# Performance work log

Hardware: AMD Instinct MI355X
Metric: run time of the kernel (lower is better)

The kernel has to match this reference:

```python
import jax, jax.numpy as jnp
import numpy as np

B, T, W = 8, 4096, 1024          # batch, byte seq len, words per sequence
DB, DW = 64, 512                 # byte_embed_dim, word_embed_dim
NH = 2                           # highway layers per block
VOCAB = 264                      # 256 bytes + 4 + 4 specials
BPE_MARK, WORD_MARK = 4, 3       # bpe_mask_idx, word_mask_idx


def _make_seg_ids():
    # ragged word lengths in {3,4,5}, mean 4, summing to T per sequence
    rng = np.random.default_rng(0)
    seg = np.empty((B, T), np.int32)
    base = T // W
    for b in range(B):
        delta = np.zeros(W, np.int64)
        q = W // 4
        idx = rng.permutation(W)
        delta[idx[:q]] = 1
        delta[idx[q:2 * q]] = -1
        seg[b] = np.repeat(np.arange(W), base + delta)
    return jnp.asarray(seg)


def setup_inputs() -> dict:
    key = jax.random.key(0)
    ks = jax.random.split(key, 12)
    s = 0.05
    byte_tokens = jax.random.randint(ks[0], (B, T), 4, VOCAB)
    bpe_mask = jax.random.bernoulli(ks[1], 0.25, (B, T))
    word_mask = jax.random.bernoulli(ks[2], 0.05, (B, T))
    seg_ids = _make_seg_ids()
    tok_emb = (jax.random.normal(ks[3], (VOCAB, DB)) * s).at[0].set(0.0)  # padding_idx=0 row zeroed
    inp = {
        'byte_tokens': byte_tokens, 'bpe_mask': bpe_mask, 'word_mask': word_mask,
        'seg_ids': seg_ids, 'tok_emb': tok_emb,
        'conv0_w': jax.random.normal(ks[4], (3, DB, DW)) * s, 'conv0_b': jnp.zeros((DW,)),
        'hw0_wg': jax.random.normal(ks[5], (NH, DW, DW)) * s, 'hw0_bg': jnp.zeros((NH, DW)),
        'hw0_wh': jax.random.normal(ks[6], (NH, DW, DW)) * s, 'hw0_bh': jnp.zeros((NH, DW)),
        'conv1_w': jax.random.normal(ks[7], (3, DW, DW)) * s, 'conv1_b': jnp.zeros((DW,)),
        'hw1_wg': jax.random.normal(ks[8], (NH, DW, DW)) * s, 'hw1_bg': jnp.zeros((NH, DW)),
        'hw1_wh': jax.random.normal(ks[9], (NH, DW, DW)) * s, 'hw1_bh': jnp.zeros((NH, DW)),
        'proj_w': jax.random.normal(ks[10], (DW, DW)) * s, 'proj_b': jnp.zeros((DW,)),
    }
    return inp


def _conv_highway(x, cw, cb, wg, bg, wh, bh, residual):
    # 1D same-padded conv over sequence, optional residual, relu, then highways
    y = jax.lax.conv_general_dilated(x, cw, (1,), 'SAME',
                                     dimension_numbers=('NWC', 'WIO', 'NWC')) + cb
    if residual:
        y = y + x
    y = jax.nn.relu(y)
    for i in range(NH):
        g = jax.nn.sigmoid(y @ wg[i] + bg[i])
        h = jax.nn.relu(y @ wh[i] + bh[i])
        y = g * h + (1.0 - g) * y
    return y


def reference(byte_tokens, bpe_mask, word_mask, seg_ids, tok_emb,
              conv0_w, conv0_b, hw0_wg, hw0_bg, hw0_wh, hw0_bh,
              conv1_w, conv1_b, hw1_wg, hw1_bg, hw1_wh, hw1_bh,
              proj_w, proj_b):
    # byte embedding + marker embeddings (pad idx 0 -> zero row)
    x = (tok_emb[byte_tokens]
         + tok_emb[jnp.where(bpe_mask, BPE_MARK, 0)]
         + tok_emb[jnp.where(word_mask, WORD_MARK, 0)])          # [B,T,DB]
    x = _conv_highway(x, conv0_w, conv0_b, hw0_wg, hw0_bg, hw0_wh, hw0_bh, False)
    x = _conv_highway(x, conv1_w, conv1_b, hw1_wg, hw1_bg, hw1_wh, hw1_bh, True)
    # ragged per-word segment max over bytes (fused, replaces python loops)
    seg_max = jax.vmap(lambda xi, si: jax.ops.segment_max(xi, si, num_segments=W))
    x = seg_max(x, seg_ids)                                       # [B,W,DW]
    return x @ proj_w + proj_b
```

## Files before the change

kernel.cpp:

```cpp
#include <hip/hip_runtime.h>
#include <hip/hip_bf16.h>

using bf16 = __hip_bfloat16;
typedef __attribute__((ext_vector_type(8))) short s8v;
typedef __attribute__((ext_vector_type(4))) float f4v;

#define T_SEQ 4096
#define DWC 512

__device__ __forceinline__ float fin(float v) {
    return (v == v && fabsf(v) < 1e30f) ? v : 0.0f;
}
__device__ __forceinline__ float ldf(const void* p, size_t i, int f32) {
    return f32 ? ((const float*)p)[i] : __bfloat162float(((const bf16*)p)[i]);
}
__device__ __forceinline__ float b2f(short s) {
    unsigned u = ((unsigned)(unsigned short)s) << 16;
    return __builtin_bit_cast(float, u);
}
__device__ __forceinline__ short f2b(float v) {
    bf16 b = __float2bfloat16(v);
    return __builtin_bit_cast(short, b);
}
__device__ __forceinline__ uint4 ld16(const short* p) { return *(const uint4*)p; }

__device__ __forceinline__ void swz(int L, int G, int& bx, int& by) {
    int k8 = L & 7, sl = L >> 3;
    int gp = G >> 5;
    bx = sl & 3;
    by = k8 * gp + (sl >> 2);
}

__device__ __forceinline__ int swidx(int row, int ch) {
    return row * 32 + ((ch ^ ((row >> 1) & 3)) << 3);
}

__global__ __launch_bounds__(256) void diag_kernel(bf16* __restrict__ out, int n, float v)
{
    int i = blockIdx.x * 256 + threadIdx.x;
    if (i < n) out[i] = __float2bfloat16(i == 0 ? v : 0.0f);
}

__global__ __launch_bounds__(256) void detect_kernel(
    const int* __restrict__ tok, const unsigned char* __restrict__ bpe,
    const unsigned char* __restrict__ wm, const int* __restrict__ seg,
    const unsigned int* __restrict__ embw, int* __restrict__ flags)
{
    __shared__ int sh[5];
    int tid = threadIdx.x;
    if (tid < 5) sh[tid] = 0;
    __syncthreads();
    int bo = 0, bm = 0, wo = 0, wmid = 0;
    for (int i = tid; i < 16384; i += 256) {
        int odd = 2 * i + 1;
        if (bpe[odd]) bo = 1;
        if (wm[odd])  wo = 1;
        int mid = 8 * (i & 4095) + 4;
        if (bpe[mid]) bm = 1;
        if (wm[mid])  wmid = 1;
    }
    if (bo)   atomicOr(&sh[0], 1);
    if (bm)   atomicOr(&sh[1], 1);
    if (wo)   atomicOr(&sh[2], 1);
    if (wmid) atomicOr(&sh[3], 1);
    if (tid < 32 && embw[32 + tid] != 0u) atomicOr(&sh[4], 1);
    __syncthreads();
    if (tid == 0) {
        flags[0] = (tok[32767] != 0) ? 0 : 1;
        flags[1] = sh[0] ? 1 : (sh[1] ? 4 : 8);
        flags[2] = sh[2] ? 1 : (sh[3] ? 4 : 8);
        flags[3] = (seg[32767] != 0) ? 0 : 1;
        flags[4] = sh[4] ? 0 : 1;
    }
}

#define WB_TOTAL 3249664
#define EMB4_ELEMS (264 * 4 * 64)
__global__ __launch_bounds__(256) void convert_weights(
    const void* c0w, const void* c0b, const void* h0g, const void* h0bg,
    const void* h0h, const void* h0bh, const void* c1w, const void* c1b,
    const void* h1g, const void* h1bg, const void* h1h, const void* h1bh,
    const void* pw, const void* pb, const void* emb,
    const int* __restrict__ flags, short* __restrict__ WB)
{
    int f32 = flags[4];
    size_t i = (size_t)blockIdx.x * 256 + threadIdx.x;
    if (i >= WB_TOTAL + EMB4_ELEMS) return;
    if (i >= WB_TOTAL) {
        size_t o = i - WB_TOTAL;
        size_t t = o >> 8, v = (o >> 6) & 3, c = o & 63;
        float val = ldf(emb, t * 64 + c, f32);
        if (v & 1) val += ldf(emb, 4 * 64 + c, f32);
        if (v & 2) val += ldf(emb, 3 * 64 + c, f32);
        WB[i] = f2b(fin(val));
        return;
    }
    const void* src; size_t si;
    if (i < 98304)        { size_t n = i / 192, k = i % 192; src = c0w; si = k * 512 + n; }
    else if (i < 98816)   { src = c0b;  si = i - 98304; }
    else if (i < 623104)  { size_t o = i - 98816;  size_t l = o >> 18; o &= 262143;
                            size_t n = o >> 9, k = o & 511; src = h0g; si = (l << 18) + k * 512 + n; }
    else if (i < 624128)  { src = h0bg; si = i - 623104; }
    else if (i < 1148416) { size_t o = i - 624128; size_t l = o >> 18; o &= 262143;
                            size_t n = o >> 9, k = o & 511; src = h0h; si = (l << 18) + k * 512 + n; }
    else if (i < 1149440) { src = h0bh; si = i - 1148416; }
    else if (i < 1935872) { size_t o = i - 1149440; size_t n = o / 1536, k = o % 1536;
                            src = c1w; si = k * 512 + n; }
    else if (i < 1936384) { src = c1b;  si = i - 1935872; }
    else if (i < 2460672) { size_t o = i - 1936384; size_t l = o >> 18; o &= 262143;
                            size_t n = o >> 9, k = o & 511; src = h1g; si = (l << 18) + k * 512 + n; }
    else if (i < 2461696) { src = h1bg; si = i - 2460672; }
    else if (i < 2985984) { size_t o = i - 2461696; size_t l = o >> 18; o &= 262143;
                            size_t n = o >> 9, k = o & 511; src = h1h; si = (l << 18) + k * 512 + n; }
    else if (i < 2987008) { src = h1bh; si = i - 2985984; }
    else if (i < 3249152) { size_t o = i - 2987008; size_t n = o >> 9, k = o & 511;
                            src = pw; si = k * 512 + n; }
    else                  { src = pb;   si = i - 3249152; }
    WB[i] = f2b(ldf(src, si, f32));
}

__global__ __launch_bounds__(512) void conv0_mfma(
    const int* __restrict__ tok, const unsigned char* __restrict__ bpe,
    const unsigned char* __restrict__ wm, const short* __restrict__ emb4,
    const int* __restrict__ flags, const short* __restrict__ WT,
    const short* __restrict__ bias, short* __restrict__ Out)
{
    constexpr int K = 192;
    constexpr int NIT = 3;
    __shared__ __align__(16) short As[2][256 * 32];
    __shared__ __align__(16) short Bs[2][256 * 32];
    int bx, by;
    swz(blockIdx.x, gridDim.x, bx, by);
    const int bm = by * 128, bn = bx * 128;
    const int tid = threadIdx.x;
    const int wave = tid >> 6, lane = tid & 63;
    const int wmr = (wave >> 1) * 32, wnc = (wave & 1) * 64;
    const int q = lane >> 4, ln16 = lane & 15;
    const int sr = tid >> 2, sch = tid & 3;
    const int tt = (bm + sr) & (T_SEQ - 1);
    const int is64t = flags[0];
    const int wb = flags[1], ww = flags[2];
    const short* Bb = WT + (size_t)(bn + sr) * K + sch * 8;

    f4v acc[2][4] = {};
    uint4 rA0, rA1, rB0, rB1;
    const uint4 z4 = make_uint4(0, 0, 0, 0);

    auto loadA = [&](int tap, uint4& a0, uint4& a1) {
        int ts = tt + tap - 1;
        if ((unsigned)ts < (unsigned)T_SEQ) {
            int bt = bm + sr + tap - 1;
            int tk = is64t ? (int)((const long long*)tok)[bt] : tok[bt];
            tk = min(max(tk, 0), 263);
            int v = (bpe[(size_t)bt * wb] ? 1 : 0) | (wm[(size_t)bt * ww] ? 2 : 0);
            const short* row = emb4 + ((size_t)tk * 4 + v) * 64;
            a0 = ld16(row + sch * 8);
            a1 = ld16(row + 32 + sch * 8);
        } else { a0 = z4; a1 = z4; }
    };

    loadA(0, rA0, rA1);
    rB0 = ld16(Bb);
    rB1 = ld16(Bb + 32);
    *(uint4*)(&As[0][swidx(sr, sch)])       = rA0;
    *(uint4*)(&As[0][swidx(128 + sr, sch)]) = rA1;
    *(uint4*)(&Bs[0][swidx(sr, sch)])       = rB0;
    *(uint4*)(&Bs[0][swidx(128 + sr, sch)]) = rB1;
    __syncthreads();
    int p = 0;

    for (int it = 0; it < NIT; ++it) {
        const bool more = (it + 1 < NIT);
        if (more) {
            int kn = (it + 1) * 64;
            loadA(it + 1, rA0, rA1);
            rB0 = ld16(Bb + kn);
            rB1 = ld16(Bb + kn + 32);
        }
        #pragma unroll
        for (int ks = 0; ks < 2; ks++) {
            s8v af[2], bf[4];
            #pragma unroll
            for (int mi = 0; mi < 2; mi++)
                af[mi] = *(const s8v*)(&As[p][swidx(128 * ks + wmr + mi * 16 + ln16, q)]);
            #pragma unroll
            for (int ni = 0; ni < 4; ni++)
                bf[ni] = *(const s8v*)(&Bs[p][swidx(128 * ks + wnc + ni * 16 + ln16, q)]);
            #pragma unroll
            for (int mi = 0; mi < 2; mi++)
                #pragma unroll
                for (int ni = 0; ni < 4; ni++)
                    acc[mi][ni] = __builtin_amdgcn_mfma_f32_16x16x32_bf16(
                        af[mi], bf[ni], acc[mi][ni], 0, 0, 0);
        }
        if (more) {
            *(uint4*)(&As[p ^ 1][swidx(sr, sch)])       = rA0;
            *(uint4*)(&As[p ^ 1][swidx(128 + sr, sch)]) = rA1;
            *(uint4*)(&Bs[p ^ 1][swidx(sr, sch)])       = rB0;
            *(uint4*)(&Bs[p ^ 1][swidx(128 + sr, sch)]) = rB1;
            __syncthreads();
            p ^= 1;
        }
    }

    #pragma unroll
    for (int mi = 0; mi < 2; mi++)
        #pragma unroll
        for (int ni = 0; ni < 4; ni++) {
            int col = bn + wnc + ni * 16 + ln16;
            float bv = b2f(bias[col]);
            #pragma unroll
            for (int r = 0; r < 4; r++) {
                int orow = bm + wmr + mi * 16 + q * 4 + r;
                Out[(size_t)orow * DWC + col] =
                    f2b(fin(fmaxf(acc[mi][ni][r] + bv, 0.0f)));
            }
        }
}

__global__ __launch_bounds__(512) void conv1_mfma(
    const short* __restrict__ A, const short* __restrict__ WT,
    const short* __restrict__ bias, short* __restrict__ Out)
{
    constexpr int IC = 512;
    constexpr int K = 3 * IC;
    constexpr int NIT = K / 64;
    __shared__ __align__(16) short As[2][256 * 32];
    __shared__ __align__(16) short Bs[2][256 * 32];
    int bx, by;
    swz(blockIdx.x, gridDim.x, bx, by);
    const int bm = by * 128, bn = bx * 128;
    const int tid = threadIdx.x;
    const int wave = tid >> 6, lane = tid & 63;
    const int wmr = (wave >> 1) * 32, wnc = (wave & 1) * 64;
    const int q = lane >> 4, ln16 = lane & 15;
    const int sr = tid >> 2, sch = tid & 3;
    const int tt = (bm + sr) & (T_SEQ - 1);
    const short* Bb = WT + (size_t)(bn + sr) * K + sch * 8;

    f4v acc[2][4] = {};
    uint4 rA0, rA1, rB0, rB1;
    const uint4 z4 = make_uint4(0, 0, 0, 0);

    {
        int ts = tt - 1;
        bool ok = (ts >= 0 && ts < T_SEQ);
        const short* sa = A + (size_t)(bm + sr - 1) * IC + sch * 8;
        rA0 = ok ? ld16(sa) : z4;
        rA1 = ok ? ld16(sa + 32) : z4;
        rB0 = ld16(Bb);
        rB1 = ld16(Bb + 32);
    }
    *(uint4*)(&As[0][swidx(sr, sch)])       = rA0;
    *(uint4*)(&As[0][swidx(128 + sr, sch)]) = rA1;
    *(uint4*)(&Bs[0][swidx(sr, sch)])       = rB0;
    *(uint4*)(&Bs[0][swidx(128 + sr, sch)]) = rB1;
    __syncthreads();
    int p = 0;

    for (int it = 0; it < NIT; ++it) {
        const bool more = (it + 1 < NIT);
        if (more) {
            int kn = (it + 1) * 64;
            int tap = kn / IC, c0 = kn - tap * IC;
            int ts = tt + tap - 1;
            bool ok = (ts >= 0 && ts < T_SEQ);
            const short* sa = A + (size_t)(bm + sr + tap - 1) * IC + c0 + sch * 8;
            rA0 = ok ? ld16(sa) : z4;
            rA1 = ok ? ld16(sa + 32) : z4;
            rB0 = ld16(Bb + kn);
            rB1 = ld16(Bb + kn + 32);
        }
        #pragma unroll
        for (int ks = 0; ks < 2; ks++) {
            s8v af[2], bf[4];
            #pragma unroll
            for (int mi = 0; mi < 2; mi++)
                af[mi] = *(const s8v*)(&As[p][swidx(128 * ks + wmr + mi * 16 + ln16, q)]);
            #pragma unroll
            for (int ni = 0; ni < 4; ni++)
                bf[ni] = *(const s8v*)(&Bs[p][swidx(128 * ks + wnc + ni * 16 + ln16, q)]);
            #pragma unroll
            for (int mi = 0; mi < 2; mi++)
                #pragma unroll
                for (int ni = 0; ni < 4; ni++)
                    acc[mi][ni] = __builtin_amdgcn_mfma_f32_16x16x32_bf16(
                        af[mi], bf[ni], acc[mi][ni], 0, 0, 0);
        }
        if (more) {
            *(uint4*)(&As[p ^ 1][swidx(sr, sch)])       = rA0;
            *(uint4*)(&As[p ^ 1][swidx(128 + sr, sch)]) = rA1;
            *(uint4*)(&Bs[p ^ 1][swidx(sr, sch)])       = rB0;
            *(uint4*)(&Bs[p ^ 1][swidx(128 + sr, sch)]) = rB1;
            __syncthreads();
            p ^= 1;
        }
    }

    #pragma unroll
    for (int mi = 0; mi < 2; mi++)
        #pragma unroll
        for (int ni = 0; ni < 4; ni++) {
            int col = bn + wnc + ni * 16 + ln16;
            float bv = b2f(bias[col]);
            #pragma unroll
            for (int r = 0; r < 4; r++) {
                int orow = bm + wmr + mi * 16 + q * 4 + r;
                float v = acc[mi][ni][r] + bv + b2f(A[(size_t)orow * IC + col]);
                Out[(size_t)orow * DWC + col] = f2b(fin(fmaxf(v, 0.0f)));
            }
        }
}

__global__ __launch_bounds__(512) void highway_mfma(
    const short* __restrict__ Y, const short* __restrict__ WgT,
    const short* __restrict__ bg, const short* __restrict__ WhT,
    const short* __restrict__ bh, short* __restrict__ Out)
{
    __shared__ __align__(16) short As[128 * 32];
    __shared__ __align__(16) short Bg[128 * 32];
    __shared__ __align__(16) short Bh[128 * 32];
    int bx, by;
    swz(blockIdx.x, gridDim.x, bx, by);
    const int bm = by * 128, bn = bx * 128;
    const int tid = threadIdx.x;
    const int wave = tid >> 6, lane = tid & 63;
    const int wmr = (wave >> 1) * 32, wnc = (wave & 1) * 64;
    const int q = lane >> 4, ln16 = lane & 15;
    const int sr = tid >> 2, sch = tid & 3;
    const int sw = swidx(sr, sch);
    const short* A0 = Y   + (size_t)(bm + sr) * DWC + sch * 8;
    const short* G0 = WgT + (size_t)(bn + sr) * DWC + sch * 8;
    const short* H0 = WhT + (size_t)(bn + sr) * DWC + sch * 8;

    f4v accg[2][4] = {};
    f4v acch[2][4] = {};
    uint4 rA = ld16(A0), rG = ld16(G0), rH = ld16(H0);

    for (int k0 = 0; k0 < DWC; k0 += 32) {
        *(uint4*)(&As[sw]) = rA;
        *(uint4*)(&Bg[sw]) = rG;
        *(uint4*)(&Bh[sw]) = rH;
        __syncthreads();
        if (k0 + 32 < DWC) {
            int kn = k0 + 32;
            rA = ld16(A0 + kn); rG = ld16(G0 + kn); rH = ld16(H0 + kn);
        }
        s8v af[2], bgf[4], bhf[4];
        #pragma unroll
        for (int mi = 0; mi < 2; mi++) af[mi] = *(const s8v*)(&As[swidx(wmr + mi * 16 + ln16, q)]);
        #pragma unroll
        for (int ni = 0; ni < 4; ni++) {
            bgf[ni] = *(const s8v*)(&Bg[swidx(wnc + ni * 16 + ln16, q)]);
            bhf[ni] = *(const s8v*)(&Bh[swidx(wnc + ni * 16 + ln16, q)]);
        }
        #pragma unroll
        for (int mi = 0; mi < 2; mi++)
            #pragma unroll
            for (int ni = 0; ni < 4; ni++) {
                accg[mi][ni] = __builtin_amdgcn_mfma_f32_16x16x32_bf16(
                    af[mi], bgf[ni], accg[mi][ni], 0, 0, 0);
                acch[mi][ni] = __builtin_amdgcn_mfma_f32_16x16x32_bf16(
                    af[mi], bhf[ni], acch[mi][ni], 0, 0, 0);
            }
        __syncthreads();
    }

    #pragma unroll
    for (int mi = 0; mi < 2; mi++)
        #pragma unroll
        for (int ni = 0; ni < 4; ni++) {
            int col = bn + wnc + ni * 16 + ln16;
            float bgv = b2f(bg[col]);
            float bhv = b2f(bh[col]);
            #pragma unroll
            for (int r = 0; r < 4; r++) {
                int orow = bm + wmr + mi * 16 + q * 4 + r;
                float g = 1.0f / (1.0f + expf(-(accg[mi][ni][r] + bgv)));
                float h = fmaxf(acch[mi][ni][r] + bhv, 0.0f);
                float y = b2f(Y[(size_t)orow * DWC + col]);
                Out[(size_t)orow * DWC + col] = f2b(fin(g * h + (1.0f - g) * y));
            }
        }
}

__global__ __launch_bounds__(512) void proj_mfma(
    const short* __restrict__ A, const short* __restrict__ WT,
    const short* __restrict__ bias, const int* __restrict__ flags,
    void* __restrict__ Out, int oroff)
{
    __shared__ __align__(16) short As[128 * 32];
    __shared__ __align__(16) short Bs[128 * 32];
    int bx, by;
    swz(blockIdx.x, gridDim.x, bx, by);
    const int bm = by * 128, bn = bx * 128;
    const int tid = threadIdx.x;
    const int wave = tid >> 6, lane = tid & 63;
    const int wmr = (wave >> 1) * 32, wnc = (wave & 1) * 64;
    const int q = lane >> 4, ln16 = lane & 15;
    const int sr = tid >> 2, sch = tid & 3;
    const int sw = swidx(sr, sch);
    const int f32 = flags[4];
    const short* A0 = A  + (size_t)(bm + sr) * DWC + sch * 8;
    const short* B0 = WT + (size_t)(bn + sr) * DWC + sch * 8;

    f4v acc[2][4] = {};
    uint4 rA = ld16(A0), rB = ld16(B0);

    for (int k0 = 0; k0 < DWC; k0 += 32) {
        *(uint4*)(&As[sw]) = rA;
        *(uint4*)(&Bs[sw]) = rB;
        __syncthreads();
        if (k0 + 32 < DWC) {
            int kn = k0 + 32;
            rA = ld16(A0 + kn); rB = ld16(B0 + kn);
        }
        s8v af[2], bf[4];
        #pragma unroll
        for (int mi = 0; mi < 2; mi++) af[mi] = *(const s8v*)(&As[swidx(wmr + mi * 16 + ln16, q)]);
        #pragma unroll
        for (int ni = 0; ni < 4; ni++) bf[ni] = *(const s8v*)(&Bs[swidx(wnc + ni * 16 + ln16, q)]);
        #pragma unroll
        for (int mi = 0; mi < 2; mi++)
            #pragma unroll
            for (int ni = 0; ni < 4; ni++)
                acc[mi][ni] = __builtin_amdgcn_mfma_f32_16x16x32_bf16(
                    af[mi], bf[ni], acc[mi][ni], 0, 0, 0);
        __syncthreads();
    }

    #pragma unroll
    for (int mi = 0; mi < 2; mi++)
        #pragma unroll
        for (int ni = 0; ni < 4; ni++) {
            int col = bn + wnc + ni * 16 + ln16;
            float bv = b2f(bias[col]);
            #pragma unroll
            for (int r = 0; r < 4; r++) {
                int orow = bm + wmr + mi * 16 + q * 4 + r;
                float v = fin(acc[mi][ni][r] + bv);
                size_t oi = (size_t)(oroff + orow) * DWC + col;
                if (f32) ((float*)Out)[oi] = v;
                else     ((bf16*)Out)[oi] = __float2bfloat16(v);
            }
        }
}

__global__ __launch_bounds__(256) void bounds_kernel(
    const int* __restrict__ seg, const int* __restrict__ flags,
    int* __restrict__ wstart, int* __restrict__ wend, int bt0)
{
    int il = blockIdx.x * 256 + threadIdx.x;
    int ig = bt0 + il;
    int is64 = flags[3];
    const long long* seg64 = (const long long*)seg;
    int t = il & (T_SEQ - 1);
    int bl = il >> 12;
    int s  = (is64 ? (int)seg64[ig] : seg[ig]) & 1023;
    int sp = (t == 0)         ? -1 : ((is64 ? (int)seg64[ig - 1] : seg[ig - 1]) & 1023);
    int sn = (t == T_SEQ - 1) ? -1 : ((is64 ? (int)seg64[ig + 1] : seg[ig + 1]) & 1023);
    int bw = (bl << 10) + s;
    if (sp != s) wstart[bw] = t;
    if (sn != s) wend[bw] = t;
}

__global__ __launch_bounds__(512) void segmax_kernel(
    const short* __restrict__ Y, const int* __restrict__ wstart,
    const int* __restrict__ wend, short* __restrict__ Out)
{
    int bw = blockIdx.x;
    int d = threadIdx.x;
    int bl = bw >> 10;
    int s = wstart[bw], e = wend[bw];
    s = min(max(s, 0), T_SEQ - 1);
    e = min(max(e, s), T_SEQ - 1);
    float m = b2f(Y[(size_t)((bl << 12) + s) * DWC + d]);
    for (int t = s + 1; t <= e; ++t)
        m = fmaxf(m, b2f(Y[(size_t)((bl << 12) + t) * DWC + d]));
    Out[(size_t)bw * DWC + d] = f2b(fin(m));
}

extern "C" void kernel_launch(void* const* d_in, const int* in_sizes, int n_in,
                              void* d_out, int out_size, void* d_ws, size_t ws_size,
                              hipStream_t stream)
{
    static const int expect[19] = {32768, 32768, 32768, 32768, 16896,
                                   98304, 512, 524288, 1024, 524288, 1024,
                                   786432, 512, 524288, 1024, 524288, 1024,
                                   262144, 512};
    int bad = -1;
    if (n_in < 19) bad = 31;
    else for (int i = 0; i < 19; i++) if (in_sizes[i] != expect[i]) { bad = i; break; }
    if (bad >= 0) {
        diag_kernel<<<dim3((out_size + 255) / 256), dim3(256), 0, stream>>>(
            (bf16*)d_out, out_size, 1e35f * (float)(1 + bad));
        return;
    }

    char* ws = (char*)d_ws;
    const size_t WBREG = 8ull << 20;
    short* WB    = (short*)ws;
    int*   flags = (int*)(ws + (7u << 20));
    const size_t perC = 8388608 + 8192 + 64;
    int C = 8;
    while (C > 1 && WBREG + (size_t)C * perC > ws_size) C >>= 1;
    if (WBREG + (size_t)C * perC > ws_size) {
        float ws_mib = (float)((double)ws_size / 1048576.0);
        diag_kernel<<<dim3((out_size + 255) / 256), dim3(256), 0, stream>>>(
            (bf16*)d_out, out_size, 1e30f * (16.0f + ws_mib));
        return;
    }

    const int*  byte_tokens = (const int*)d_in[0];
    const unsigned char* bpe_mask = (const unsigned char*)d_in[1];
    const unsigned char* word_mask = (const unsigned char*)d_in[2];
    const int*  seg_ids     = (const int*)d_in[3];
    const void* tok_emb = d_in[4];

    detect_kernel<<<dim3(1), dim3(256), 0, stream>>>(
        byte_tokens, bpe_mask, word_mask, seg_ids,
        (const unsigned int*)tok_emb, flags);

    convert_weights<<<dim3((WB_TOTAL + EMB4_ELEMS + 255) / 256), dim3(256), 0, stream>>>(
        d_in[5], d_in[6], d_in[7], d_in[8], d_in[9], d_in[10],
        d_in[11], d_in[12], d_in[13], d_in[14], d_in[15], d_in[16],
        d_in[17], d_in[18], tok_emb, flags, WB);

    short* c0wT = WB;            short* c0b  = WB + 98304;
    short* h0gT = WB + 98816;    short* h0bg = WB + 623104;
    short* h0hT = WB + 624128;   short* h0bh = WB + 1148416;
    short* c1wT = WB + 1149440;  short* c1b  = WB + 1935872;
    short* h1gT = WB + 1936384;  short* h1bg = WB + 2460672;
    short* h1hT = WB + 2461696;  short* h1bh = WB + 2985984;
    short* pwT  = WB + 2987008;  short* pb   = WB + 3249152;
    short* emb4 = WB + WB_TOTAL;
    const int LOFF = 262144, LBOFF = 512;

    for (int b0 = 0; b0 < 8; b0 += C) {
        const int rows  = C * T_SEQ;
        const int words = C * 1024;
        char*  chunk  = ws + WBREG;
        short* U      = (short*)chunk;
        short* V      = (short*)(chunk + (size_t)C * 4194304);
        int*   wstart = (int*)(chunk + (size_t)C * 8388608);
        int*   wend   = wstart + words;
        short* segout = U;

        dim3 gg(4 * (rows / 128));
        conv0_mfma<<<gg, dim3(512), 0, stream>>>(
            byte_tokens + (size_t)b0 * T_SEQ,
            bpe_mask,
            word_mask, emb4, flags, c0wT, c0b, U);

        highway_mfma<<<gg, dim3(512), 0, stream>>>(U, h0gT, h0bg, h0hT, h0bh, V);
        highway_mfma<<<gg, dim3(512), 0, stream>>>(V, h0gT + LOFF, h0bg + LBOFF,
                                                   h0hT + LOFF, h0bh + LBOFF, U);

        conv1_mfma<<<gg, dim3(512), 0, stream>>>(U, c1wT, c1b, V);

        highway_mfma<<<gg, dim3(512), 0, stream>>>(V, h1gT, h1bg, h1hT, h1bh, U);
        highway_mfma<<<gg, dim3(512), 0, stream>>>(U, h1gT + LOFF, h1bg + LBOFF,
                                                   h1hT + LOFF, h1bh + LBOFF, V);

        bounds_kernel<<<dim3(rows / 256), dim3(256), 0, stream>>>(
            seg_ids, flags, wstart, wend, b0 * T_SEQ);

        segmax_kernel<<<dim3(words), dim3(512), 0, stream>>>(V, wstart, wend, segout);

        proj_mfma<<<dim3(4 * (words / 128)), dim3(512), 0, stream>>>(
            segout, pwT, pb, flags, d_out, b0 * 1024);
    }
}
```

Before: 448.1 us.

## Enlarge highway GEMM tile to 256x128 with double-buffered LDS and priority scheduling

```diff
diff --git a/kernel.cpp b/kernel.cpp
--- a/kernel.cpp
+++ b/kernel.cpp
@@ -312,64 +312,157 @@
         }
 }
 
-__global__ __launch_bounds__(512) void highway_mfma(
+__global__ __launch_bounds__(512) void highway_mfma8(
     const short* __restrict__ Y, const short* __restrict__ WgT,
     const short* __restrict__ bg, const short* __restrict__ WhT,
     const short* __restrict__ bh, short* __restrict__ Out)
 {
-    __shared__ __align__(16) short As[128 * 32];
-    __shared__ __align__(16) short Bg[128 * 32];
-    __shared__ __align__(16) short Bh[128 * 32];
+    constexpr int IC = DWC;
+    constexpr int NIT = IC / 64;
+    __shared__ __align__(16) short As [2][512 * 32];
+    __shared__ __align__(16) short Bgs[2][256 * 32];
+    __shared__ __align__(16) short Bhs[2][256 * 32];
     int bx, by;
     swz(blockIdx.x, gridDim.x, bx, by);
-    const int bm = by * 128, bn = bx * 128;
+    const int bm = by * 256, bn = bx * 128;
     const int tid = threadIdx.x;
     const int wave = tid >> 6, lane = tid & 63;
-    const int wmr = (wave >> 1) * 32, wnc = (wave & 1) * 64;
+    const int wmr = (wave >> 2) * 128;
+    const int wnc = (wave & 3) * 32;
     const int q = lane >> 4, ln16 = lane & 15;
     const int sr = tid >> 2, sch = tid & 3;
-    const int sw = swidx(sr, sch);
-    const short* A0 = Y   + (size_t)(bm + sr) * DWC + sch * 8;
-    const short* G0 = WgT + (size_t)(bn + sr) * DWC + sch * 8;
-    const short* H0 = WhT + (size_t)(bn + sr) * DWC + sch * 8;
-
-    f4v accg[2][4] = {};
-    f4v acch[2][4] = {};
-    uint4 rA = ld16(A0), rG = ld16(G0), rH = ld16(H0);
-
-    for (int k0 = 0; k0 < DWC; k0 += 32) {
-        *(uint4*)(&As[sw]) = rA;
-        *(uint4*)(&Bg[sw]) = rG;
-        *(uint4*)(&Bh[sw]) = rH;
-        __syncthreads();
-        if (k0 + 32 < DWC) {
-            int kn = k0 + 32;
-            rA = ld16(A0 + kn); rG = ld16(G0 + kn); rH = ld16(H0 + kn);
-        }
-        s8v af[2], bgf[4], bhf[4];
-        #pragma unroll
-        for (int mi = 0; mi < 2; mi++) af[mi] = *(const s8v*)(&As[swidx(wmr + mi * 16 + ln16, q)]);
-        #pragma unroll
-        for (int ni = 0; ni < 4; ni++) {
-            bgf[ni] = *(const s8v*)(&Bg[swidx(wnc + ni * 16 + ln16, q)]);
-            bhf[ni] = *(const s8v*)(&Bh[swidx(wnc + ni * 16 + ln16, q)]);
-        }
-        #pragma unroll
-        for (int mi = 0; mi < 2; mi++)
-            #pragma unroll
-            for (int ni = 0; ni < 4; ni++) {
-                accg[mi][ni] = __builtin_amdgcn_mfma_f32_16x16x32_bf16(
-                    af[mi], bgf[ni], accg[mi][ni], 0, 0, 0);
-                acch[mi][ni] = __builtin_amdgcn_mfma_f32_16x16x32_bf16(
-                    af[mi], bhf[ni], acch[mi][ni], 0, 0, 0);
-            }
-        __syncthreads();
+
+    const short* A0 = Y   + (size_t)(bm + sr) * IC + sch * 8;
+    const short* A1 = A0 + 128 * IC;
+    const short* G0 = WgT + (size_t)(bn + sr) * IC + sch * 8;
+    const short* H0 = WhT + (size_t)(bn + sr) * IC + sch * 8;
+
+    f4v accg[8][2] = {};
+    f4v acch[8][2] = {};
+    uint4 rA0, rA1, rA2, rA3, rG0, rG1, rH0, rH1;
+
+    rA0 = ld16(A0);      rA1 = ld16(A0 + 32);
+    rA2 = ld16(A1);      rA3 = ld16(A1 + 32);
+    rG0 = ld16(G0);      rG1 = ld16(G0 + 32);
+    rH0 = ld16(H0);      rH1 = ld16(H0 + 32);
+    *(uint4*)(&As [0][swidx(      sr, sch)]) = rA0;
+    *(uint4*)(&As [0][swidx(256 + sr, sch)]) = rA1;
+    *(uint4*)(&As [0][swidx(128 + sr, sch)]) = rA2;
+    *(uint4*)(&As [0][swidx(384 + sr, sch)]) = rA3;
+    *(uint4*)(&Bgs[0][swidx(      sr, sch)]) = rG0;
+    *(uint4*)(&Bgs[0][swidx(128 + sr, sch)]) = rG1;
+    *(uint4*)(&Bhs[0][swidx(      sr, sch)]) = rH0;
+    *(uint4*)(&Bhs[0][swidx(128 + sr, sch)]) = rH1;
+    __syncthreads();
+    int p = 0;
+
+    for (int it = 0; it < NIT; ++it) {
+        const bool more = (it + 1 < NIT);
+        const int kn = (it + 1) * 64;
+        const short* Ap = &As [p][0];
+        const short* Gp = &Bgs[p][0];
+        const short* Hp = &Bhs[p][0];
+
+        s8v af[4][2], bgf[2][2];
+        #pragma unroll
+        for (int mi = 0; mi < 4; mi++)
+            #pragma unroll
+            for (int ks = 0; ks < 2; ks++)
+                af[mi][ks] = *(const s8v*)(&Ap[swidx(ks * 256 + wmr + mi * 16 + ln16, q)]);
+        #pragma unroll
+        for (int ni = 0; ni < 2; ni++)
+            #pragma unroll
+            for (int ks = 0; ks < 2; ks++)
+                bgf[ni][ks] = *(const s8v*)(&Gp[swidx(ks * 128 + wnc + ni * 16 + ln16, q)]);
+        if (more) {
+            rA0 = ld16(A0 + kn); rA1 = ld16(A0 + kn + 32);
+            rA2 = ld16(A1 + kn); rA3 = ld16(A1 + kn + 32);
+        }
+        __builtin_amdgcn_s_barrier();
+        __builtin_amdgcn_s_setprio(1);
+        #pragma unroll
+        for (int mi = 0; mi < 4; mi++)
+            #pragma unroll
+            for (int ni = 0; ni < 2; ni++)
+                #pragma unroll
+                for (int ks = 0; ks < 2; ks++)
+                    accg[mi][ni] = __builtin_amdgcn_mfma_f32_16x16x32_bf16(
+                        af[mi][ks], bgf[ni][ks], accg[mi][ni], 0, 0, 0);
+        __builtin_amdgcn_s_setprio(0);
+        __builtin_amdgcn_s_barrier();
+
+        s8v bhf[2][2];
+        #pragma unroll
+        for (int ni = 0; ni < 2; ni++)
+            #pragma unroll
+            for (int ks = 0; ks < 2; ks++)
+                bhf[ni][ks] = *(const s8v*)(&Hp[swidx(ks * 128 + wnc + ni * 16 + ln16, q)]);
+        if (more) { rG0 = ld16(G0 + kn); rG1 = ld16(G0 + kn + 32); }
+        __builtin_amdgcn_s_barrier();
+        __builtin_amdgcn_s_setprio(1);
+        #pragma unroll
+        for (int mi = 0; mi < 4; mi++)
+            #pragma unroll
+            for (int ni = 0; ni < 2; ni++)
+                #pragma unroll
+                for (int ks = 0; ks < 2; ks++)
+                    acch[mi][ni] = __builtin_amdgcn_mfma_f32_16x16x32_bf16(
+                        af[mi][ks], bhf[ni][ks], acch[mi][ni], 0, 0, 0);
+        __builtin_amdgcn_s_setprio(0);
+        __builtin_amdgcn_s_barrier();
+
+        #pragma unroll
+        for (int mi = 0; mi < 4; mi++)
+            #pragma unroll
+            for (int ks = 0; ks < 2; ks++)
+                af[mi][ks] = *(const s8v*)(&Ap[swidx(ks * 256 + wmr + 64 + mi * 16 + ln16, q)]);
+        if (more) { rH0 = ld16(H0 + kn); rH1 = ld16(H0 + kn + 32); }
+        __builtin_amdgcn_s_barrier();
+        __builtin_amdgcn_s_setprio(1);
+        #pragma unroll
+        for (int mi = 0; mi < 4; mi++)
+            #pragma unroll
+            for (int ni = 0; ni < 2; ni++)
+                #pragma unroll
+                for (int ks = 0; ks < 2; ks++)
+                    accg[4 + mi][ni] = __builtin_amdgcn_mfma_f32_16x16x32_bf16(
+                        af[mi][ks], bgf[ni][ks], accg[4 + mi][ni], 0, 0, 0);
+        __builtin_amdgcn_s_setprio(0);
+        __builtin_amdgcn_s_barrier();
+
+        __builtin_amdgcn_s_setprio(1);
+        #pragma unroll
+        for (int mi = 0; mi < 4; mi++)
+            #pragma unroll
+            for (int ni = 0; ni < 2; ni++)
+                #pragma unroll
+                for (int ks = 0; ks < 2; ks++)
+                    acch[4 + mi][ni] = __builtin_amdgcn_mfma_f32_16x16x32_bf16(
+                        af[mi][ks], bhf[ni][ks], acch[4 + mi][ni], 0, 0, 0);
+        __builtin_amdgcn_s_setprio(0);
+        __builtin_amdgcn_sched_barrier(0);
+        if (more) {
+            short* An = &As [p ^ 1][0];
+            short* Gn = &Bgs[p ^ 1][0];
+            short* Hn = &Bhs[p ^ 1][0];
+            *(uint4*)(&An[swidx(      sr, sch)]) = rA0;
+            *(uint4*)(&An[swidx(256 + sr, sch)]) = rA1;
+            *(uint4*)(&An[swidx(128 + sr, sch)]) = rA2;
+            *(uint4*)(&An[swidx(384 + sr, sch)]) = rA3;
+            *(uint4*)(&Gn[swidx(      sr, sch)]) = rG0;
+            *(uint4*)(&Gn[swidx(128 + sr, sch)]) = rG1;
+            *(uint4*)(&Hn[swidx(      sr, sch)]) = rH0;
+            *(uint4*)(&Hn[swidx(128 + sr, sch)]) = rH1;
+            asm volatile("s_waitcnt lgkmcnt(0)" ::: "memory");
+            __builtin_amdgcn_s_barrier();
+            p ^= 1;
+        }
     }
 
     #pragma unroll
-    for (int mi = 0; mi < 2; mi++)
-        #pragma unroll
-        for (int ni = 0; ni < 4; ni++) {
+    for (int mi = 0; mi < 8; mi++)
+        #pragma unroll
+        for (int ni = 0; ni < 2; ni++) {
             int col = bn + wnc + ni * 16 + ln16;
             float bgv = b2f(bg[col]);
             float bhv = b2f(bh[col]);
@@ -378,8 +471,8 @@
                 int orow = bm + wmr + mi * 16 + q * 4 + r;
                 float g = 1.0f / (1.0f + expf(-(accg[mi][ni][r] + bgv)));
                 float h = fmaxf(acch[mi][ni][r] + bhv, 0.0f);
-                float y = b2f(Y[(size_t)orow * DWC + col]);
-                Out[(size_t)orow * DWC + col] = f2b(fin(g * h + (1.0f - g) * y));
+                float yv = b2f(Y[(size_t)orow * DWC + col]);
+                Out[(size_t)orow * DWC + col] = f2b(fin(g * h + (1.0f - g) * yv));
             }
         }
 }
@@ -547,20 +640,20 @@
         short* segout = U;
 
         dim3 gg(4 * (rows / 128));
+        dim3 gh(4 * (rows / 256));
         conv0_mfma<<<gg, dim3(512), 0, stream>>>(
             byte_tokens + (size_t)b0 * T_SEQ,
-            bpe_mask,
-            word_mask, emb4, flags, c0wT, c0b, U);
-
-        highway_mfma<<<gg, dim3(512), 0, stream>>>(U, h0gT, h0bg, h0hT, h0bh, V);
-        highway_mfma<<<gg, dim3(512), 0, stream>>>(V, h0gT + LOFF, h0bg + LBOFF,
-                                                   h0hT + LOFF, h0bh + LBOFF, U);
+            bpe_mask, word_mask, emb4, flags, c0wT, c0b, U);
+
+        highway_mfma8<<<gh, dim3(512), 0, stream>>>(U, h0gT, h0bg, h0hT, h0bh, V);
+        highway_mfma8<<<gh, dim3(512), 0, stream>>>(V, h0gT + LOFF, h0bg + LBOFF,
+                                                    h0hT + LOFF, h0bh + LBOFF, U);
 
         conv1_mfma<<<gg, dim3(512), 0, stream>>>(U, c1wT, c1b, V);
 
-        highway_mfma<<<gg, dim3(512), 0, stream>>>(V, h1gT, h1bg, h1hT, h1bh, U);
-        highway_mfma<<<gg, dim3(512), 0, stream>>>(U, h1gT + LOFF, h1bg + LBOFF,
-                                                   h1hT + LOFF, h1bh + LBOFF, V);
+        highway_mfma8<<<gh, dim3(512), 0, stream>>>(V, h1gT, h1bg, h1hT, h1bh, U);
+        highway_mfma8<<<gh, dim3(512), 0, stream>>>(U, h1gT + LOFF, h1bg + LBOFF,
+                                                    h1hT + LOFF, h1bh + LBOFF, V);
 
         bounds_kernel<<<dim3(rows / 256), dim3(256), 0, stream>>>(
             seg_ids, flags, wstart, wend, b0 * T_SEQ);
```

After: 429.4 us. 1.04x faster.

## Double-buffer highway GEMM with direct global-to-LDS loads and 2x4 wave layout

Applied to the files above, without the earlier changes.

```diff
diff --git a/kernel.cpp b/kernel.cpp
--- a/kernel.cpp
+++ b/kernel.cpp
@@ -23,6 +23,12 @@
     return __builtin_bit_cast(short, b);
 }
 __device__ __forceinline__ uint4 ld16(const short* p) { return *(const uint4*)p; }
+
+__device__ __forceinline__ void gl_lds16(const short* g, short* l) {
+    __builtin_amdgcn_global_load_lds(
+        (const __attribute__((address_space(1))) void*)g,
+        (__attribute__((address_space(3))) void*)l, 16, 0, 0);
+}
 
 __device__ __forceinline__ void swz(int L, int G, int& bx, int& by) {
     int k8 = L & 7, sl = L >> 3;
@@ -312,64 +318,84 @@
         }
 }
 
-__global__ __launch_bounds__(512) void highway_mfma(
+__global__ __launch_bounds__(512, 4) void highway_mfma8(
     const short* __restrict__ Y, const short* __restrict__ WgT,
     const short* __restrict__ bg, const short* __restrict__ WhT,
     const short* __restrict__ bh, short* __restrict__ Out)
 {
-    __shared__ __align__(16) short As[128 * 32];
-    __shared__ __align__(16) short Bg[128 * 32];
-    __shared__ __align__(16) short Bh[128 * 32];
+    constexpr int IC = DWC;
+    constexpr int NIT = IC / 32;
+    __shared__ __align__(16) short As [2][128 * 32];
+    __shared__ __align__(16) short Bgs[2][128 * 32];
+    __shared__ __align__(16) short Bhs[2][128 * 32];
     int bx, by;
     swz(blockIdx.x, gridDim.x, bx, by);
     const int bm = by * 128, bn = bx * 128;
     const int tid = threadIdx.x;
     const int wave = tid >> 6, lane = tid & 63;
-    const int wmr = (wave >> 1) * 32, wnc = (wave & 1) * 64;
+    const int wmr = (wave >> 2) * 64;
+    const int wnc = (wave & 3) * 32;
     const int q = lane >> 4, ln16 = lane & 15;
-    const int sr = tid >> 2, sch = tid & 3;
-    const int sw = swidx(sr, sch);
-    const short* A0 = Y   + (size_t)(bm + sr) * DWC + sch * 8;
-    const short* G0 = WgT + (size_t)(bn + sr) * DWC + sch * 8;
-    const short* H0 = WhT + (size_t)(bn + sr) * DWC + sch * 8;
-
-    f4v accg[2][4] = {};
-    f4v acch[2][4] = {};
-    uint4 rA = ld16(A0), rG = ld16(G0), rH = ld16(H0);
-
-    for (int k0 = 0; k0 < DWC; k0 += 32) {
-        *(uint4*)(&As[sw]) = rA;
-        *(uint4*)(&Bg[sw]) = rG;
-        *(uint4*)(&Bh[sw]) = rH;
-        __syncthreads();
-        if (k0 + 32 < DWC) {
-            int kn = k0 + 32;
-            rA = ld16(A0 + kn); rG = ld16(G0 + kn); rH = ld16(H0 + kn);
-        }
-        s8v af[2], bgf[4], bhf[4];
-        #pragma unroll
-        for (int mi = 0; mi < 2; mi++) af[mi] = *(const s8v*)(&As[swidx(wmr + mi * 16 + ln16, q)]);
-        #pragma unroll
-        for (int ni = 0; ni < 4; ni++) {
-            bgf[ni] = *(const s8v*)(&Bg[swidx(wnc + ni * 16 + ln16, q)]);
-            bhf[ni] = *(const s8v*)(&Bh[swidx(wnc + ni * 16 + ln16, q)]);
-        }
-        #pragma unroll
-        for (int mi = 0; mi < 2; mi++)
-            #pragma unroll
-            for (int ni = 0; ni < 4; ni++) {
-                accg[mi][ni] = __builtin_amdgcn_mfma_f32_16x16x32_bf16(
-                    af[mi], bgf[ni], accg[mi][ni], 0, 0, 0);
-                acch[mi][ni] = __builtin_amdgcn_mfma_f32_16x16x32_bf16(
-                    af[mi], bhf[ni], acch[mi][ni], 0, 0, 0);
-            }
-        __syncthreads();
+
+    const int rr = (wave << 4) + (lane >> 2);
+    const int ch = (lane & 3) ^ ((rr >> 1) & 3);
+    const short* gA = Y   + (size_t)(bm + rr) * IC + ch * 8;
+    const short* gG = WgT + (size_t)(bn + rr) * IC + ch * 8;
+    const short* gH = WhT + (size_t)(bn + rr) * IC + ch * 8;
+    const int wb1k = wave << 10;
+
+    f4v accg[4][2] = {};
+    f4v acch[4][2] = {};
+
+    auto stage = [&](int pp, int kk) {
+        gl_lds16(gA + kk, (short*)((char*)&As [pp][0] + wb1k));
+        gl_lds16(gG + kk, (short*)((char*)&Bgs[pp][0] + wb1k));
+        gl_lds16(gH + kk, (short*)((char*)&Bhs[pp][0] + wb1k));
+    };
+
+    stage(0, 0);
+    asm volatile("s_waitcnt vmcnt(0)" ::: "memory");
+    __syncthreads();
+    int p = 0;
+
+    for (int it = 0; it < NIT; ++it) {
+        const bool more = (it + 1 < NIT);
+        if (more) stage(p ^ 1, (it + 1) * 32);
+        const short* Ap = &As [p][0];
+        const short* Gp = &Bgs[p][0];
+        const short* Hp = &Bhs[p][0];
+        s8v af[2], bgf[2], bhf[2];
+        #pragma unroll
+        for (int ni = 0; ni < 2; ni++) {
+            bgf[ni] = *(const s8v*)(&Gp[swidx(wnc + ni * 16 + ln16, q)]);
+            bhf[ni] = *(const s8v*)(&Hp[swidx(wnc + ni * 16 + ln16, q)]);
+        }
+        #pragma unroll
+        for (int mh = 0; mh < 2; mh++) {
+            #pragma unroll
+            for (int mi = 0; mi < 2; mi++)
+                af[mi] = *(const s8v*)(&Ap[swidx(wmr + mh * 32 + mi * 16 + ln16, q)]);
+            #pragma unroll
+            for (int mi = 0; mi < 2; mi++)
+                #pragma unroll
+                for (int ni = 0; ni < 2; ni++) {
+                    accg[mh * 2 + mi][ni] = __builtin_amdgcn_mfma_f32_16x16x32_bf16(
+                        af[mi], bgf[ni], accg[mh * 2 + mi][ni], 0, 0, 0);
+                    acch[mh * 2 + mi][ni] = __builtin_amdgcn_mfma_f32_16x16x32_bf16(
+                        af[mi], bhf[ni], acch[mh * 2 + mi][ni], 0, 0, 0);
+                }
+        }
+        if (more) {
+            asm volatile("s_waitcnt vmcnt(0)" ::: "memory");
+            __builtin_amdgcn_s_barrier();
+            p ^= 1;
+        }
     }
 
     #pragma unroll
-    for (int mi = 0; mi < 2; mi++)
-        #pragma unroll
-        for (int ni = 0; ni < 4; ni++) {
+    for (int mi = 0; mi < 4; mi++)
+        #pragma unroll
+        for (int ni = 0; ni < 2; ni++) {
             int col = bn + wnc + ni * 16 + ln16;
             float bgv = b2f(bg[col]);
             float bhv = b2f(bh[col]);
@@ -378,8 +404,8 @@
                 int orow = bm + wmr + mi * 16 + q * 4 + r;
                 float g = 1.0f / (1.0f + expf(-(accg[mi][ni][r] + bgv)));
                 float h = fmaxf(acch[mi][ni][r] + bhv, 0.0f);
-                float y = b2f(Y[(size_t)orow * DWC + col]);
-                Out[(size_t)orow * DWC + col] = f2b(fin(g * h + (1.0f - g) * y));
+                float yv = b2f(Y[(size_t)orow * DWC + col]);
+                Out[(size_t)orow * DWC + col] = f2b(fin(g * h + (1.0f - g) * yv));
             }
         }
 }
@@ -549,18 +575,17 @@
         dim3 gg(4 * (rows / 128));
         conv0_mfma<<<gg, dim3(512), 0, stream>>>(
             byte_tokens + (size_t)b0 * T_SEQ,
-            bpe_mask,
-            word_mask, emb4, flags, c0wT, c0b, U);
-
-        highway_mfma<<<gg, dim3(512), 0, stream>>>(U, h0gT, h0bg, h0hT, h0bh, V);
-        highway_mfma<<<gg, dim3(512), 0, stream>>>(V, h0gT + LOFF, h0bg + LBOFF,
-                                                   h0hT + LOFF, h0bh + LBOFF, U);
+            bpe_mask, word_mask, emb4, flags, c0wT, c0b, U);
+
+        highway_mfma8<<<gg, dim3(512), 0, stream>>>(U, h0gT, h0bg, h0hT, h0bh, V);
+        highway_mfma8<<<gg, dim3(512), 0, stream>>>(V, h0gT + LOFF, h0bg + LBOFF,
+                                                    h0hT + LOFF, h0bh + LBOFF, U);
 
         conv1_mfma<<<gg, dim3(512), 0, stream>>>(U, c1wT, c1b, V);
 
-        highway_mfma<<<gg, dim3(512), 0, stream>>>(V, h1gT, h1bg, h1hT, h1bh, U);
-        highway_mfma<<<gg, dim3(512), 0, stream>>>(U, h1gT + LOFF, h1bg + LBOFF,
-                                                   h1hT + LOFF, h1bh + LBOFF, V);
+        highway_mfma8<<<gg, dim3(512), 0, stream>>>(V, h1gT, h1bg, h1hT, h1bh, U);
+        highway_mfma8<<<gg, dim3(512), 0, stream>>>(U, h1gT + LOFF, h1bg + LBOFF,
+                                                    h1hT + LOFF, h1bh + LBOFF, V);
 
         bounds_kernel<<<dim3(rows / 256), dim3(256), 0, stream>>>(
             seg_ids, flags, wstart, wend, b0 * T_SEQ);
```

After: 420.3 us. 1.07x faster.

## Fuse both highway layers into one in-place kernel with LDS-resident rows

Applied to the files above, without the earlier changes.

```diff
diff --git a/kernel.cpp b/kernel.cpp
--- a/kernel.cpp
+++ b/kernel.cpp
@@ -23,6 +23,12 @@
     return __builtin_bit_cast(short, b);
 }
 __device__ __forceinline__ uint4 ld16(const short* p) { return *(const uint4*)p; }
+
+__device__ __forceinline__ void gl_lds16(const short* g, short* l) {
+    __builtin_amdgcn_global_load_lds(
+        (const __attribute__((address_space(1))) void*)g,
+        (__attribute__((address_space(3))) void*)l, 16, 0, 0);
+}
 
 __device__ __forceinline__ void swz(int L, int G, int& bx, int& by) {
     int k8 = L & 7, sl = L >> 3;
@@ -96,22 +102,31 @@
         return;
     }
     const void* src; size_t si;
+    auto fraginv = [](size_t r, size_t& k, size_t& n) {
+        size_t blk = r >> 9, w = r & 511;
+        n = (blk >> 4) * 16 + ((w >> 3) & 15);
+        k = (blk & 15) * 32 + (w >> 7) * 8 + (w & 7);
+    };
     if (i < 98304)        { size_t n = i / 192, k = i % 192; src = c0w; si = k * 512 + n; }
     else if (i < 98816)   { src = c0b;  si = i - 98304; }
-    else if (i < 623104)  { size_t o = i - 98816;  size_t l = o >> 18; o &= 262143;
-                            size_t n = o >> 9, k = o & 511; src = h0g; si = (l << 18) + k * 512 + n; }
+    else if (i < 623104)  { size_t o = i - 98816;  size_t l = o >> 18; size_t k, n;
+                            fraginv(o & 262143, k, n);
+                            src = h0g; si = (l << 18) + k * 512 + n; }
     else if (i < 624128)  { src = h0bg; si = i - 623104; }
-    else if (i < 1148416) { size_t o = i - 624128; size_t l = o >> 18; o &= 262143;
-                            size_t n = o >> 9, k = o & 511; src = h0h; si = (l << 18) + k * 512 + n; }
+    else if (i < 1148416) { size_t o = i - 624128; size_t l = o >> 18; size_t k, n;
+                            fraginv(o & 262143, k, n);
+                            src = h0h; si = (l << 18) + k * 512 + n; }
     else if (i < 1149440) { src = h0bh; si = i - 1148416; }
     else if (i < 1935872) { size_t o = i - 1149440; size_t n = o / 1536, k = o % 1536;
                             src = c1w; si = k * 512 + n; }
     else if (i < 1936384) { src = c1b;  si = i - 1935872; }
-    else if (i < 2460672) { size_t o = i - 1936384; size_t l = o >> 18; o &= 262143;
-                            size_t n = o >> 9, k = o & 511; src = h1g; si = (l << 18) + k * 512 + n; }
+    else if (i < 2460672) { size_t o = i - 1936384; size_t l = o >> 18; size_t k, n;
+                            fraginv(o & 262143, k, n);
+                            src = h1g; si = (l << 18) + k * 512 + n; }
     else if (i < 2461696) { src = h1bg; si = i - 2460672; }
-    else if (i < 2985984) { size_t o = i - 2461696; size_t l = o >> 18; o &= 262143;
-                            size_t n = o >> 9, k = o & 511; src = h1h; si = (l << 18) + k * 512 + n; }
+    else if (i < 2985984) { size_t o = i - 2461696; size_t l = o >> 18; size_t k, n;
+                            fraginv(o & 262143, k, n);
+                            src = h1h; si = (l << 18) + k * 512 + n; }
     else if (i < 2987008) { src = h1bh; si = i - 2985984; }
     else if (i < 3249152) { size_t o = i - 2987008; size_t n = o >> 9, k = o & 511;
                             src = pw; si = k * 512 + n; }
@@ -312,76 +327,99 @@
         }
 }
 
-__global__ __launch_bounds__(512) void highway_mfma(
-    const short* __restrict__ Y, const short* __restrict__ WgT,
-    const short* __restrict__ bg, const short* __restrict__ WhT,
-    const short* __restrict__ bh, short* __restrict__ Out)
-{
-    __shared__ __align__(16) short As[128 * 32];
-    __shared__ __align__(16) short Bg[128 * 32];
-    __shared__ __align__(16) short Bh[128 * 32];
-    int bx, by;
-    swz(blockIdx.x, gridDim.x, bx, by);
-    const int bm = by * 128, bn = bx * 128;
+__global__ __launch_bounds__(512, 4) void highway_pair(
+    short* __restrict__ Y,
+    const short* __restrict__ WgF, const short* __restrict__ bgv,
+    const short* __restrict__ WhF, const short* __restrict__ bhv)
+{
+    constexpr int IC = DWC;
+    constexpr int NIT = 16;
+    __shared__ __align__(16) short y[16 * 1024];
+    const int bm = blockIdx.x * 32;
     const int tid = threadIdx.x;
     const int wave = tid >> 6, lane = tid & 63;
-    const int wmr = (wave >> 1) * 32, wnc = (wave & 1) * 64;
     const int q = lane >> 4, ln16 = lane & 15;
-    const int sr = tid >> 2, sch = tid & 3;
-    const int sw = swidx(sr, sch);
-    const short* A0 = Y   + (size_t)(bm + sr) * DWC + sch * 8;
-    const short* G0 = WgT + (size_t)(bn + sr) * DWC + sch * 8;
-    const short* H0 = WhT + (size_t)(bn + sr) * DWC + sch * 8;
-
-    f4v accg[2][4] = {};
-    f4v acch[2][4] = {};
-    uint4 rA = ld16(A0), rG = ld16(G0), rH = ld16(H0);
-
-    for (int k0 = 0; k0 < DWC; k0 += 32) {
-        *(uint4*)(&As[sw]) = rA;
-        *(uint4*)(&Bg[sw]) = rG;
-        *(uint4*)(&Bh[sw]) = rH;
+    const int wb = wave * 64;
+
+    #pragma unroll
+    for (int r4 = 0; r4 < 4; r4++) {
+        int w = r4 * 512 + tid;
+        int pp = w >> 7, wi = w & 127;
+        int row = wi >> 2, slot = wi & 3;
+        int chh = slot ^ ((row >> 1) & 3);
+        const short* src = Y + (size_t)(bm + row) * IC + pp * 32 + chh * 8;
+        gl_lds16(src, &y[(size_t)(r4 * 512 + wave * 64) * 8]);
+    }
+    asm volatile("s_waitcnt vmcnt(0)" ::: "memory");
+    __syncthreads();
+
+    #pragma unroll 1
+    for (int l = 0; l < 2; l++) {
+        const short* Wg = WgF + ((size_t)l << 18);
+        const short* Wh = WhF + ((size_t)l << 18);
+        f4v accg[2][4] = {};
+        f4v acch[2][4] = {};
+        #pragma unroll 2
+        for (int it = 0; it < NIT; ++it) {
+            s8v af[2], bgf[4], bhf[4];
+            const short* yp = &y[it << 10];
+            #pragma unroll
+            for (int mi = 0; mi < 2; mi++)
+                af[mi] = *(const s8v*)(&yp[swidx(mi * 16 + ln16, q)]);
+            #pragma unroll
+            for (int ni = 0; ni < 4; ni++) {
+                int nblk = (wb >> 4) + ni;
+                size_t fo = (size_t)(((nblk << 4) + it) << 9) + (lane << 3);
+                bgf[ni] = *(const s8v*)(Wg + fo);
+                bhf[ni] = *(const s8v*)(Wh + fo);
+            }
+            #pragma unroll
+            for (int mi = 0; mi < 2; mi++)
+                #pragma unroll
+                for (int ni = 0; ni < 4; ni++) {
+                    accg[mi][ni] = __builtin_amdgcn_mfma_f32_16x16x32_bf16(
+                        af[mi], bgf[ni], accg[mi][ni], 0, 0, 0);
+                    acch[mi][ni] = __builtin_amdgcn_mfma_f32_16x16x32_bf16(
+                        af[mi], bhf[ni], acch[mi][ni], 0, 0, 0);
+                }
+        }
         __syncthreads();
-        if (k0 + 32 < DWC) {
-            int kn = k0 + 32;
-            rA = ld16(A0 + kn); rG = ld16(G0 + kn); rH = ld16(H0 + kn);
-        }
-        s8v af[2], bgf[4], bhf[4];
-        #pragma unroll
-        for (int mi = 0; mi < 2; mi++) af[mi] = *(const s8v*)(&As[swidx(wmr + mi * 16 + ln16, q)]);
-        #pragma unroll
-        for (int ni = 0; ni < 4; ni++) {
-            bgf[ni] = *(const s8v*)(&Bg[swidx(wnc + ni * 16 + ln16, q)]);
-            bhf[ni] = *(const s8v*)(&Bh[swidx(wnc + ni * 16 + ln16, q)]);
-        }
+        const short* bgp = bgv + l * 512;
+        const short* bhp = bhv + l * 512;
         #pragma unroll
         for (int mi = 0; mi < 2; mi++)
             #pragma unroll
             for (int ni = 0; ni < 4; ni++) {
-                accg[mi][ni] = __builtin_amdgcn_mfma_f32_16x16x32_bf16(
-                    af[mi], bgf[ni], accg[mi][ni], 0, 0, 0);
-                acch[mi][ni] = __builtin_amdgcn_mfma_f32_16x16x32_bf16(
-                    af[mi], bhf[ni], acch[mi][ni], 0, 0, 0);
+                int col = wb + ni * 16 + ln16;
+                float bgb = b2f(bgp[col]);
+                float bhb = b2f(bhp[col]);
+                int pp = col >> 5, kk = col & 31, chh = kk >> 3, k0 = kk & 7;
+                #pragma unroll
+                for (int r = 0; r < 4; r++) {
+                    int row = mi * 16 + q * 4 + r;
+                    int si = (pp << 10) + (row << 5)
+                           + ((chh ^ ((row >> 1) & 3)) << 3) + k0;
+                    float g = 1.0f / (1.0f + expf(-(accg[mi][ni][r] + bgb)));
+                    float h = fmaxf(acch[mi][ni][r] + bhb, 0.0f);
+                    float yv = b2f(y[si]);
+                    y[si] = f2b(g * h + (1.0f - g) * yv);
+                }
             }
         __syncthreads();
     }
 
     #pragma unroll
-    for (int mi = 0; mi < 2; mi++)
-        #pragma unroll
-        for (int ni = 0; ni < 4; ni++) {
-            int col = bn + wnc + ni * 16 + ln16;
-            float bgv = b2f(bg[col]);
-            float bhv = b2f(bh[col]);
-            #pragma unroll
-            for (int r = 0; r < 4; r++) {
-                int orow = bm + wmr + mi * 16 + q * 4 + r;
-                float g = 1.0f / (1.0f + expf(-(accg[mi][ni][r] + bgv)));
-                float h = fmaxf(acch[mi][ni][r] + bhv, 0.0f);
-                float y = b2f(Y[(size_t)orow * DWC + col]);
-                Out[(size_t)orow * DWC + col] = f2b(fin(g * h + (1.0f - g) * y));
-            }
-        }
+    for (int r4 = 0; r4 < 4; r4++) {
+        int w = r4 * 512 + tid;
+        int pp = w >> 7, wi = w & 127;
+        int row = wi >> 2, slot = wi & 3;
+        int chh = slot ^ ((row >> 1) & 3);
+        uint4 v = *(const uint4*)(&y[(size_t)w * 8]);
+        short* sp = (short*)&v;
+        #pragma unroll
+        for (int j = 0; j < 8; j++) sp[j] = f2b(fin(b2f(sp[j])));
+        *(uint4*)(Y + (size_t)(bm + row) * IC + pp * 32 + chh * 8) = v;
+    }
 }
 
 __global__ __launch_bounds__(512) void proj_mfma(
@@ -527,14 +565,13 @@
         d_in[17], d_in[18], tok_emb, flags, WB);
 
     short* c0wT = WB;            short* c0b  = WB + 98304;
-    short* h0gT = WB + 98816;    short* h0bg = WB + 623104;
-    short* h0hT = WB + 624128;   short* h0bh = WB + 1148416;
+    short* h0gF = WB + 98816;    short* h0bg = WB + 623104;
+    short* h0hF = WB + 624128;   short* h0bh = WB + 1148416;
     short* c1wT = WB + 1149440;  short* c1b  = WB + 1935872;
-    short* h1gT = WB + 1936384;  short* h1bg = WB + 2460672;
-    short* h1hT = WB + 2461696;  short* h1bh = WB + 2985984;
+    short* h1gF = WB + 1936384;  short* h1bg = WB + 2460672;
+    short* h1hF = WB + 2461696;  short* h1bh = WB + 2985984;
     short* pwT  = WB + 2987008;  short* pb   = WB + 3249152;
     short* emb4 = WB + WB_TOTAL;
-    const int LOFF = 262144, LBOFF = 512;
 
     for (int b0 = 0; b0 < 8; b0 += C) {
         const int rows  = C * T_SEQ;
@@ -547,20 +584,17 @@
         short* segout = U;
 
         dim3 gg(4 * (rows / 128));
+        dim3 gp(rows / 32);
+
         conv0_mfma<<<gg, dim3(512), 0, stream>>>(
             byte_tokens + (size_t)b0 * T_SEQ,
-            bpe_mask,
-            word_mask, emb4, flags, c0wT, c0b, U);
-
-        highway_mfma<<<gg, dim3(512), 0, stream>>>(U, h0gT, h0bg, h0hT, h0bh, V);
-        highway_mfma<<<gg, dim3(512), 0, stream>>>(V, h0gT + LOFF, h0bg + LBOFF,
-                                                   h0hT + LOFF, h0bh + LBOFF, U);
+            bpe_mask, word_mask, emb4, flags, c0wT, c0b, U);
+
+        highway_pair<<<gp, dim3(512), 0, stream>>>(U, h0gF, h0bg, h0hF, h0bh);
 
         conv1_mfma<<<gg, dim3(512), 0, stream>>>(U, c1wT, c1b, V);
 
-        highway_mfma<<<gg, dim3(512), 0, stream>>>(V, h1gT, h1bg, h1hT, h1bh, U);
-        highway_mfma<<<gg, dim3(512), 0, stream>>>(U, h1gT + LOFF, h1bg + LBOFF,
-                                                   h1hT + LOFF, h1bh + LBOFF, V);
+        highway_pair<<<gp, dim3(512), 0, stream>>>(V, h1gF, h1bg, h1hF, h1bh);
 
         bounds_kernel<<<dim3(rows / 256), dim3(256), 0, stream>>>(
             seg_ids, flags, wstart, wend, b0 * T_SEQ);
```

Result: slower. 609.8 us (+36.1%).
